# Optimization experiments

Hardware: AMD Instinct MI355X
Metric: run time of the kernel (lower is better)

The kernel has to match this reference:

```python
import jax, jax.numpy as jnp
import numpy as np

B, S, D = 1, 4096, 768
H = 12
HD = D // H  # 64


def setup_inputs() -> dict:
    key = jax.random.key(0)
    ks = jax.random.split(key, 6)
    sd = 1.0 / np.sqrt(D)
    return {
        "inputs": jax.random.normal(ks[0], (B, S, D), dtype=jnp.float32),
        "Wq": jax.random.uniform(ks[1], (D, D), jnp.float32, -sd, sd),
        "Wk": jax.random.uniform(ks[2], (D, D), jnp.float32, -sd, sd),
        "Wv": jax.random.uniform(ks[3], (D, D), jnp.float32, -sd, sd),
        "Wo": jax.random.uniform(ks[4], (D, D), jnp.float32, -sd, sd),
        "bo": jax.random.uniform(ks[5], (D,), jnp.float32, -sd, sd),
    }


def reference(inputs, Wq, Wk, Wv, Wo, bo):
    b, n, _ = inputs.shape
    # Linear layers (torch Linear: x @ W.T); W stored as [d_out, d_in]-equivalent here as [D, D] applied via x @ W.T
    q = inputs @ Wq.T  # [b, n, D]
    k = inputs @ Wk.T
    v = inputs @ Wv.T
    # [b, H, n, HD]
    q = q.reshape(b, n, H, HD).transpose(0, 2, 1, 3)
    k = k.reshape(b, n, H, HD).transpose(0, 2, 1, 3)
    v = v.reshape(b, n, H, HD).transpose(0, 2, 1, 3)
    scores = jnp.einsum("bhqd,bhkd->bhqk", q, k)
    causal = jnp.triu(jnp.ones((n, n), dtype=bool), k=1)
    scores = jnp.where(causal, -jnp.inf, scores)
    attn = jax.nn.softmax(scores / np.sqrt(HD), axis=-1)  # dropout p=0.0 -> identity
    ctx = jnp.einsum("bhqk,bhkd->bhqd", attn, v)
    ctx = ctx.transpose(0, 2, 1, 3).reshape(b, n, D)
    return ctx @ Wo.T + bo
```

## Files before the change

kernel.cpp:

```cpp
#include <hip/hip_runtime.h>
#include <math.h>

static constexpr int S_LEN  = 4096;
static constexpr int DMODEL = 768;
static constexpr int NHEAD  = 12;
static constexpr int HDIM   = 64;

typedef __attribute__((ext_vector_type(8))) short   bf16x8;
typedef __attribute__((ext_vector_type(4))) float   f32x4;
typedef __attribute__((ext_vector_type(8))) unsigned short us8;

__device__ __forceinline__ unsigned short f2b(float f) {
  union { float f; unsigned int u; } v; v.f = f;
  unsigned int u = v.u;
  return (unsigned short)((u + 0x7fffu + ((u >> 16) & 1u)) >> 16);
}

__device__ __forceinline__ unsigned short f2b_fast(float f) {
  unsigned int u;
  asm("v_cvt_pk_bf16_f32 %0, %1, %2" : "=v"(u) : "v"(f), "v"(0.f));
  return (unsigned short)u;
}

__device__ __forceinline__ float dpp_max16(float x) {
  float y;
  y = __int_as_float(__builtin_amdgcn_mov_dpp(__float_as_int(x), 0xB1, 0xf, 0xf, true)); x = fmaxf(x, y);
  y = __int_as_float(__builtin_amdgcn_mov_dpp(__float_as_int(x), 0x4E, 0xf, 0xf, true)); x = fmaxf(x, y);
  y = __int_as_float(__builtin_amdgcn_mov_dpp(__float_as_int(x), 0x124, 0xf, 0xf, true)); x = fmaxf(x, y);
  y = __int_as_float(__builtin_amdgcn_mov_dpp(__float_as_int(x), 0x128, 0xf, 0xf, true)); x = fmaxf(x, y);
  return x;
}

__global__ __launch_bounds__(256)
void cvt_f2b_kern(const float* __restrict__ in, unsigned short* __restrict__ out, int n) {
  int i = (blockIdx.x * blockDim.x + threadIdx.x) * 8;
  if (i >= n) return;
  float4 a = *(const float4*)(in + i);
  float4 b = *(const float4*)(in + i + 4);
  ushort4 o0; o0.x = f2b(a.x); o0.y = f2b(a.y); o0.z = f2b(a.z); o0.w = f2b(a.w);
  ushort4 o1; o1.x = f2b(b.x); o1.y = f2b(b.y); o1.z = f2b(b.z); o1.w = f2b(b.w);
  *(ushort4*)(out + i)     = o0;
  *(ushort4*)(out + i + 4) = o1;
}

__global__ __launch_bounds__(256)
void cvt_f2b4_kern(const float* __restrict__ s0, const float* __restrict__ s1,
                   const float* __restrict__ s2, const float* __restrict__ s3,
                   unsigned short* __restrict__ d0, unsigned short* __restrict__ d1,
                   unsigned short* __restrict__ d2, unsigned short* __restrict__ d3,
                   int n) {
  const float* s; unsigned short* d;
  switch (blockIdx.y) {
    case 0: s = s0; d = d0; break;
    case 1: s = s1; d = d1; break;
    case 2: s = s2; d = d2; break;
    default: s = s3; d = d3; break;
  }
  int i = (blockIdx.x * blockDim.x + threadIdx.x) * 8;
  if (i >= n) return;
  float4 a = *(const float4*)(s + i);
  float4 b = *(const float4*)(s + i + 4);
  ushort4 o0; o0.x = f2b(a.x); o0.y = f2b(a.y); o0.z = f2b(a.z); o0.w = f2b(a.w);
  ushort4 o1; o1.x = f2b(b.x); o1.y = f2b(b.y); o1.z = f2b(b.z); o1.w = f2b(b.w);
  *(ushort4*)(d + i)     = o0;
  *(ushort4*)(d + i + 4) = o1;
}

__global__ __launch_bounds__(256)
void transpose_bf16(const unsigned short* __restrict__ in, unsigned short* __restrict__ out) {
  __shared__ __align__(16) unsigned short Ts[64][72];
  const int d0 = blockIdx.x * 64, s0 = blockIdx.y * 64;
  const int r = threadIdx.x >> 2, q = threadIdx.x & 3;
#pragma unroll
  for (int hh = 0; hh < 2; ++hh) {
    const int c8 = q + hh * 4;
    us8 v = *(const us8*)(in + (size_t)(s0 + r) * DMODEL + d0 + c8 * 8);
    *(us8*)(&Ts[r][c8 * 8]) = v;
  }
  __syncthreads();
#pragma unroll
  for (int hh = 0; hh < 2; ++hh) {
    const int sq = q + hh * 4;
    __align__(16) unsigned short tmp[8];
#pragma unroll
    for (int j = 0; j < 8; ++j) tmp[j] = Ts[sq * 8 + j][r];
    *(us8*)(out + (size_t)(d0 + r) * S_LEN + s0 + sq * 8) = *(us8*)tmp;
  }
}

template<int OUT_MODE>
__device__ __forceinline__
void gemm_body(const unsigned short* __restrict__ A, const unsigned short* __restrict__ B,
               const float* __restrict__ bias, void* __restrict__ Cout,
               int M, int N, int K, float scale, int bx, int by,
               unsigned short* As, unsigned short* Bs) {
  const int l  = threadIdx.x & 63;
  const int w  = threadIdx.x >> 6;
  const int wm = (w >> 1) * 32, wn = (w & 1) * 32;
  const int m0 = by * 64;
  const int n0 = bx * 64;
  const int lr = l & 15, lg = l >> 4;
  const int sr = threadIdx.x >> 2, sq = threadIdx.x & 3;

  f32x4 acc[2][2] = {};
  us8 areg[2], breg[2];

#pragma unroll
  for (int p = 0; p < 2; ++p) {
    const int c = sq * 2 + p;
    areg[p] = *(const us8*)(A + (size_t)(m0 + sr) * K + c * 8);
    breg[p] = *(const us8*)(B + (size_t)(n0 + sr) * K + c * 8);
  }
#pragma unroll
  for (int p = 0; p < 2; ++p) {
    const int c = sq * 2 + p;
    const int slot = ((c ^ (sr & 7)) * 8);
    *(us8*)(&As[sr * 64 + slot]) = areg[p];
    *(us8*)(&Bs[sr * 64 + slot]) = breg[p];
  }
  __syncthreads();

  const int nsteps = K / 64;
  for (int t = 0; t < nsteps; ++t) {
    const bool more = (t + 1 < nsteps);
    if (more) {
      const int kn = (t + 1) * 64;
#pragma unroll
      for (int p = 0; p < 2; ++p) {
        const int c = sq * 2 + p;
        areg[p] = *(const us8*)(A + (size_t)(m0 + sr) * K + kn + c * 8);
        breg[p] = *(const us8*)(B + (size_t)(n0 + sr) * K + kn + c * 8);
      }
    }
#pragma unroll
    for (int kc = 0; kc < 2; ++kc) {
      const int cr = kc * 4 + lg;
      bf16x8 af[2], bfr[2];
#pragma unroll
      for (int mi = 0; mi < 2; ++mi) {
        const int row = wm + mi * 16 + lr;
        af[mi] = *(const bf16x8*)(&As[row * 64 + ((cr ^ (row & 7)) * 8)]);
      }
#pragma unroll
      for (int ni = 0; ni < 2; ++ni) {
        const int row = wn + ni * 16 + lr;
        bfr[ni] = *(const bf16x8*)(&Bs[row * 64 + ((cr ^ (row & 7)) * 8)]);
      }
#pragma unroll
      for (int mi = 0; mi < 2; ++mi)
#pragma unroll
        for (int ni = 0; ni < 2; ++ni)
          acc[mi][ni] = __builtin_amdgcn_mfma_f32_16x16x32_bf16(af[mi], bfr[ni], acc[mi][ni], 0, 0, 0);
    }
    __syncthreads();
    if (more) {
#pragma unroll
      for (int p = 0; p < 2; ++p) {
        const int c = sq * 2 + p;
        const int slot = ((c ^ (sr & 7)) * 8);
        *(us8*)(&As[sr * 64 + slot]) = areg[p];
        *(us8*)(&Bs[sr * 64 + slot]) = breg[p];
      }
      __syncthreads();
    }
  }

  const int orow = (l >> 4) * 4;
#pragma unroll
  for (int mi = 0; mi < 2; ++mi)
#pragma unroll
    for (int ni = 0; ni < 2; ++ni) {
      const int col = n0 + wn + ni * 16 + lr;
      float bb = (OUT_MODE == 1) ? bias[col] : 0.f;
#pragma unroll
      for (int r = 0; r < 4; ++r) {
        const int row = m0 + wm + mi * 16 + orow + r;
        float v = acc[mi][ni][r] * scale;
        if (OUT_MODE == 0)
          ((unsigned short*)Cout)[(size_t)row * N + col] = f2b(v);
        else
          ((float*)Cout)[(size_t)row * N + col] = v + bb;
      }
    }
}

__global__ __launch_bounds__(256)
void gemm_qkv_lds(const unsigned short* __restrict__ X,
                  const unsigned short* __restrict__ Wq, const unsigned short* __restrict__ Wk,
                  const unsigned short* __restrict__ Wv,
                  unsigned short* __restrict__ Qh, unsigned short* __restrict__ Kh,
                  unsigned short* __restrict__ Vh) {
  __shared__ __align__(16) unsigned short As[64 * 64];
  __shared__ __align__(16) unsigned short Bs[64 * 64];
  const unsigned short* B; unsigned short* C; float scale;
  switch (blockIdx.z) {
    case 0:  B = Wq; C = Qh; scale = 0.125f * 1.4426950408889634f; break;
    case 1:  B = Wk; C = Kh; scale = 1.0f;   break;
    default: B = Wv; C = Vh; scale = 1.0f;   break;
  }
  gemm_body<0>(X, B, nullptr, C, S_LEN, DMODEL, DMODEL, scale,
               blockIdx.x, blockIdx.y, As, Bs);
}

__global__ __launch_bounds__(256)
void gemm_lds_f32(const unsigned short* __restrict__ A, const unsigned short* __restrict__ B,
                  const float* __restrict__ bias, float* __restrict__ C) {
  __shared__ __align__(16) unsigned short As[64 * 64];
  __shared__ __align__(16) unsigned short Bs[64 * 64];
  gemm_body<1>(A, B, bias, C, S_LEN, DMODEL, DMODEL, 1.0f,
               blockIdx.x, blockIdx.y, As, Bs);
}

__global__ __launch_bounds__(256, 3)
void attn_fwd_mfma(const unsigned short* __restrict__ Q, const unsigned short* __restrict__ K,
                   const unsigned short* __restrict__ Vt, unsigned short* __restrict__ O) {
  __shared__ __align__(16) unsigned short Ks[2][64 * 64];
  __shared__ __align__(16) unsigned short Vs[2][64 * 64];
  __shared__ __align__(16) unsigned short Ps[4][2 * 16 * 64];

  const int item = blockIdx.x;
  int s;
  if (item < 256)      s = item;
  else if (item < 512) s = 767 - item;
  else                 s = item;
  const int qt = 63 - s / NHEAD;
  const int h  = s % NHEAD;
  const int q0 = qt * 64;
  const int tid = threadIdx.x;
  const int w = tid >> 6, l = tid & 63;
  const int lr = l & 15, lg = l >> 4;
  const int sr = tid >> 2, sq = tid & 3;

  const bf16x8 ones = {(short)0x3F80, (short)0x3F80, (short)0x3F80, (short)0x3F80,
                       (short)0x3F80, (short)0x3F80, (short)0x3F80, (short)0x3F80};

  bf16x8 qf[2];
#pragma unroll
  for (int kc = 0; kc < 2; ++kc)
    qf[kc] = *(const bf16x8*)(Q + (size_t)(q0 + w * 16 + lr) * DMODEL + h * HDIM + kc * 32 + lg * 8);

  f32x4 o_acc[4] = {};
  f32x4 l_acc = {};
  float m_i[4];
#pragma unroll
  for (int r = 0; r < 4; ++r) m_i[r] = -1e30f;

  const int nt2    = (qt + 2) >> 1;
  const int ntFull = (64 * qt >= 127) ? ((64 * qt - 127) / 128 + 1) : 0;

  us8 kreg[2][2], vreg[2][2];

#pragma unroll
  for (int hh = 0; hh < 2; ++hh)
#pragma unroll
    for (int p = 0; p < 2; ++p) {
      const int qw = sq * 2 + p;
      kreg[hh][p] = *(const us8*)(K  + (size_t)(hh * 64 + sr) * DMODEL + h * HDIM + qw * 8);
      vreg[hh][p] = *(const us8*)(Vt + (size_t)(h * HDIM + sr) * S_LEN + hh * 64 + qw * 8);
    }
#pragma unroll
  for (int hh = 0; hh < 2; ++hh)
#pragma unroll
    for (int p = 0; p < 2; ++p) {
      const int qw = sq * 2 + p;
      const int sw = (qw * 8) ^ ((sr & 7) * 8);
      *(us8*)(&Ks[hh][sr * 64 + sw]) = kreg[hh][p];
      *(us8*)(&Vs[hh][sr * 64 + sw]) = vreg[hh][p];
    }
  __syncthreads();

  for (int t = 0; t < nt2; ++t) {
    const int k0 = t * 128;
    const bool more = (t + 1 < nt2);
    const bool need_mask = (t >= ntFull);

    if (more) {
      const int k0n = k0 + 128;
#pragma unroll
      for (int hh = 0; hh < 2; ++hh)
#pragma unroll
        for (int p = 0; p < 2; ++p) {
          const int qw = sq * 2 + p;
          kreg[hh][p] = *(const us8*)(K  + (size_t)(k0n + hh * 64 + sr) * DMODEL + h * HDIM + qw * 8);
          vreg[hh][p] = *(const us8*)(Vt + (size_t)(h * HDIM + sr) * S_LEN + k0n + hh * 64 + qw * 8);
        }
    }

    f32x4 sacc[2][4] = {};
    __builtin_amdgcn_s_setprio(1);
#pragma unroll
    for (int hh = 0; hh < 2; ++hh)
#pragma unroll
      for (int kc = 0; kc < 2; ++kc)
#pragma unroll
        for (int cb = 0; cb < 4; ++cb) {
          const int kv = cb * 16 + lr;
          bf16x8 kf = *(const bf16x8*)(&Ks[hh][kv * 64 + ((kc * 32 + lg * 8) ^ ((kv & 7) * 8))]);
          sacc[hh][cb] = __builtin_amdgcn_mfma_f32_16x16x32_bf16(qf[kc], kf, sacc[hh][cb], 0, 0, 0);
        }
    __builtin_amdgcn_s_setprio(0);

    float sv[4][8], pm[4];
#pragma unroll
    for (int r = 0; r < 4; ++r) {
      const int qg = q0 + w * 16 + lg * 4 + r;
#pragma unroll
      for (int hh = 0; hh < 2; ++hh)
#pragma unroll
        for (int cb = 0; cb < 4; ++cb)
          sv[r][hh * 4 + cb] = sacc[hh][cb][r];
      if (need_mask) {
#pragma unroll
        for (int hh = 0; hh < 2; ++hh)
#pragma unroll
          for (int cb = 0; cb < 4; ++cb) {
            const int kg = k0 + hh * 64 + cb * 16 + lr;
            if (kg > qg) sv[r][hh * 4 + cb] = -1e30f;
          }
      }
      float mt = fmaxf(fmaxf(fmaxf(sv[r][0], sv[r][1]), fmaxf(sv[r][2], sv[r][3])),
                       fmaxf(fmaxf(sv[r][4], sv[r][5]), fmaxf(sv[r][6], sv[r][7])));
      pm[r] = dpp_max16(mt);
    }

    const int ok = (pm[0] <= m_i[0] + 8.f) && (pm[1] <= m_i[1] + 8.f) &&
                   (pm[2] <= m_i[2] + 8.f) && (pm[3] <= m_i[3] + 8.f);
    if (!__all(ok)) {
#pragma unroll
      for (int r = 0; r < 4; ++r) {
        const float mnew = fmaxf(m_i[r], pm[r]);
        const float alpha = __builtin_amdgcn_exp2f(m_i[r] - mnew);
        m_i[r] = mnew;
        l_acc[r] *= alpha;
#pragma unroll
        for (int db = 0; db < 4; ++db) o_acc[db][r] *= alpha;
      }
    }

    float p[4][8];
#pragma unroll
    for (int r = 0; r < 4; ++r)
#pragma unroll
      for (int e = 0; e < 8; ++e)
        p[r][e] = __builtin_amdgcn_exp2f(sv[r][e] - m_i[r]);

#pragma unroll
    for (int r = 0; r < 4; ++r) {
      const int qloc = lg * 4 + r;
#pragma unroll
      for (int hh = 0; hh < 2; ++hh)
#pragma unroll
        for (int cb = 0; cb < 4; ++cb) {
          const int kvl = cb * 16 + lr;
          Ps[w][hh * 1024 + qloc * 64 + (kvl ^ ((qloc & 7) * 8))] = f2b_fast(p[r][hh * 4 + cb]);
        }
    }

    __builtin_amdgcn_s_setprio(1);
#pragma unroll
    for (int hh = 0; hh < 2; ++hh)
#pragma unroll
      for (int kc = 0; kc < 2; ++kc) {
        bf16x8 pf = *(const bf16x8*)(&Ps[w][hh * 1024 + lr * 64 + ((kc * 32 + lg * 8) ^ ((lr & 7) * 8))]);
#pragma unroll
        for (int db = 0; db < 4; ++db) {
          const int d = db * 16 + lr;
          bf16x8 vf = *(const bf16x8*)(&Vs[hh][d * 64 + ((kc * 32 + lg * 8) ^ ((d & 7) * 8))]);
          o_acc[db] = __builtin_amdgcn_mfma_f32_16x16x32_bf16(pf, vf, o_acc[db], 0, 0, 0);
        }
        l_acc = __builtin_amdgcn_mfma_f32_16x16x32_bf16(pf, ones, l_acc, 0, 0, 0);
      }
    __builtin_amdgcn_s_setprio(0);

    __syncthreads();
    if (more) {
#pragma unroll
      for (int hh = 0; hh < 2; ++hh)
#pragma unroll
        for (int p = 0; p < 2; ++p) {
          const int qw = sq * 2 + p;
          const int sw = (qw * 8) ^ ((sr & 7) * 8);
          *(us8*)(&Ks[hh][sr * 64 + sw]) = kreg[hh][p];
          *(us8*)(&Vs[hh][sr * 64 + sw]) = vreg[hh][p];
        }
      __syncthreads();
    }
  }

#pragma unroll
  for (int r = 0; r < 4; ++r) {
    const float inv = 1.f / l_acc[r];
    const int row = q0 + w * 16 + lg * 4 + r;
#pragma unroll
    for (int db = 0; db < 4; ++db)
      O[(size_t)row * DMODEL + h * HDIM + db * 16 + lr] = f2b_fast(o_acc[db][r] * inv);
  }
}

extern "C" void kernel_launch(void* const* d_in, const int* in_sizes, int n_in,
                              void* d_out, int out_size, void* d_ws, size_t ws_size,
                              hipStream_t stream) {
  const float* x  = (const float*)d_in[0];
  const float* Wq = (const float*)d_in[1];
  const float* Wk = (const float*)d_in[2];
  const float* Wv = (const float*)d_in[3];
  const float* Wo = (const float*)d_in[4];
  const float* bo = (const float*)d_in[5];
  float* out = (float*)d_out;

  const size_t SD = (size_t)S_LEN * DMODEL;
  const size_t DD = (size_t)DMODEL * DMODEL;

  unsigned short* xh   = (unsigned short*)d_ws;
  unsigned short* Wqh  = xh   + SD;
  unsigned short* Wkh  = Wqh  + DD;
  unsigned short* Wvh  = Wkh  + DD;
  unsigned short* Woh  = Wvh  + DD;
  unsigned short* Qh   = Woh  + DD;
  unsigned short* Kh   = Qh   + SD;
  unsigned short* Vh   = Kh   + SD;
  unsigned short* Vth  = Vh   + SD;
  unsigned short* ctxh = Vth  + SD;

  const dim3 blk(256);

  cvt_f2b_kern<<<dim3((int)(SD / 8 / 256)), blk, 0, stream>>>(x, xh, (int)SD);
  cvt_f2b4_kern<<<dim3((int)(DD / 8 / 256), 4), blk, 0, stream>>>(
      Wq, Wk, Wv, Wo, Wqh, Wkh, Wvh, Woh, (int)DD);

  gemm_qkv_lds<<<dim3(DMODEL / 64, S_LEN / 64, 3), blk, 0, stream>>>(
      xh, Wqh, Wkh, Wvh, Qh, Kh, Vh);

  transpose_bf16<<<dim3(DMODEL / 64, S_LEN / 64), blk, 0, stream>>>(Vh, Vth);

  attn_fwd_mfma<<<dim3(S_LEN / 64 * NHEAD), blk, 0, stream>>>(Qh, Kh, Vth, ctxh);

  gemm_lds_f32<<<dim3(DMODEL / 64, S_LEN / 64), blk, 0, stream>>>(ctxh, Woh, bo, out);
}
```

Measured before the change: 135.0 us.

## Keep attention P in registers via transposed S MFMA and lane shuffles

Result: slower. 176.7 us (+30.9%).

```diff
diff --git a/kernel.cpp b/kernel.cpp
--- a/kernel.cpp
+++ b/kernel.cpp
@@ -21,14 +21,10 @@
   asm("v_cvt_pk_bf16_f32 %0, %1, %2" : "=v"(u) : "v"(f), "v"(0.f));
   return (unsigned short)u;
 }
-
-__device__ __forceinline__ float dpp_max16(float x) {
-  float y;
-  y = __int_as_float(__builtin_amdgcn_mov_dpp(__float_as_int(x), 0xB1, 0xf, 0xf, true)); x = fmaxf(x, y);
-  y = __int_as_float(__builtin_amdgcn_mov_dpp(__float_as_int(x), 0x4E, 0xf, 0xf, true)); x = fmaxf(x, y);
-  y = __int_as_float(__builtin_amdgcn_mov_dpp(__float_as_int(x), 0x124, 0xf, 0xf, true)); x = fmaxf(x, y);
-  y = __int_as_float(__builtin_amdgcn_mov_dpp(__float_as_int(x), 0x128, 0xf, 0xf, true)); x = fmaxf(x, y);
-  return x;
+__device__ __forceinline__ unsigned int cvt_pk(float lo, float hi) {
+  unsigned int u;
+  asm("v_cvt_pk_bf16_f32 %0, %1, %2" : "=v"(u) : "v"(lo), "v"(hi));
+  return u;
 }
 
 __global__ __launch_bounds__(256)
@@ -211,12 +207,11 @@
                blockIdx.x, blockIdx.y, As, Bs);
 }
 
-__global__ __launch_bounds__(256, 3)
+__global__ __launch_bounds__(256, 5)
 void attn_fwd_mfma(const unsigned short* __restrict__ Q, const unsigned short* __restrict__ K,
                    const unsigned short* __restrict__ Vt, unsigned short* __restrict__ O) {
   __shared__ __align__(16) unsigned short Ks[2][64 * 64];
   __shared__ __align__(16) unsigned short Vs[2][64 * 64];
-  __shared__ __align__(16) unsigned short Ps[4][2 * 16 * 64];
 
   const int item = blockIdx.x;
   int s;
@@ -230,9 +225,8 @@
   const int w = tid >> 6, l = tid & 63;
   const int lr = l & 15, lg = l >> 4;
   const int sr = tid >> 2, sq = tid & 3;
-
-  const bf16x8 ones = {(short)0x3F80, (short)0x3F80, (short)0x3F80, (short)0x3F80,
-                       (short)0x3F80, (short)0x3F80, (short)0x3F80, (short)0x3F80};
+  const bool hiP = (lg >= 2);
+  const bool hiQ = (lg & 1) != 0;
 
   bf16x8 qf[2];
 #pragma unroll
@@ -240,10 +234,8 @@
     qf[kc] = *(const bf16x8*)(Q + (size_t)(q0 + w * 16 + lr) * DMODEL + h * HDIM + kc * 32 + lg * 8);
 
   f32x4 o_acc[4] = {};
-  f32x4 l_acc = {};
-  float m_i[4];
-#pragma unroll
-  for (int r = 0; r < 4; ++r) m_i[r] = -1e30f;
+  float m_i = -1e30f, l_i = 0.f;
+  const int qg = q0 + w * 16 + lr;
 
   const int nt2    = (qt + 2) >> 1;
   const int ntFull = (64 * qt >= 127) ? ((64 * qt - 127) / 128 + 1) : 0;
@@ -296,80 +288,103 @@
         for (int cb = 0; cb < 4; ++cb) {
           const int kv = cb * 16 + lr;
           bf16x8 kf = *(const bf16x8*)(&Ks[hh][kv * 64 + ((kc * 32 + lg * 8) ^ ((kv & 7) * 8))]);
-          sacc[hh][cb] = __builtin_amdgcn_mfma_f32_16x16x32_bf16(qf[kc], kf, sacc[hh][cb], 0, 0, 0);
+          sacc[hh][cb] = __builtin_amdgcn_mfma_f32_16x16x32_bf16(kf, qf[kc], sacc[hh][cb], 0, 0, 0);
         }
     __builtin_amdgcn_s_setprio(0);
 
-    float sv[4][8], pm[4];
-#pragma unroll
-    for (int r = 0; r < 4; ++r) {
-      const int qg = q0 + w * 16 + lg * 4 + r;
+    if (need_mask) {
 #pragma unroll
       for (int hh = 0; hh < 2; ++hh)
 #pragma unroll
         for (int cb = 0; cb < 4; ++cb)
-          sv[r][hh * 4 + cb] = sacc[hh][cb][r];
-      if (need_mask) {
-#pragma unroll
-        for (int hh = 0; hh < 2; ++hh)
-#pragma unroll
-          for (int cb = 0; cb < 4; ++cb) {
-            const int kg = k0 + hh * 64 + cb * 16 + lr;
-            if (kg > qg) sv[r][hh * 4 + cb] = -1e30f;
+#pragma unroll
+          for (int r = 0; r < 4; ++r) {
+            const int kg = k0 + hh * 64 + cb * 16 + lg * 4 + r;
+            if (kg > qg) sacc[hh][cb][r] = -1e30f;
           }
-      }
-      float mt = fmaxf(fmaxf(fmaxf(sv[r][0], sv[r][1]), fmaxf(sv[r][2], sv[r][3])),
-                       fmaxf(fmaxf(sv[r][4], sv[r][5]), fmaxf(sv[r][6], sv[r][7])));
-      pm[r] = dpp_max16(mt);
-    }
-
-    const int ok = (pm[0] <= m_i[0] + 8.f) && (pm[1] <= m_i[1] + 8.f) &&
-                   (pm[2] <= m_i[2] + 8.f) && (pm[3] <= m_i[3] + 8.f);
+    }
+
+    float mx = -1e30f;
+#pragma unroll
+    for (int hh = 0; hh < 2; ++hh)
+#pragma unroll
+      for (int cb = 0; cb < 4; ++cb) {
+        float a = fmaxf(sacc[hh][cb][0], sacc[hh][cb][1]);
+        float b = fmaxf(sacc[hh][cb][2], sacc[hh][cb][3]);
+        mx = fmaxf(mx, fmaxf(a, b));
+      }
+    mx = fmaxf(mx, __shfl_xor(mx, 16));
+    mx = fmaxf(mx, __shfl_xor(mx, 32));
+
+    const int ok = (mx <= m_i + 8.f);
     if (!__all(ok)) {
-#pragma unroll
-      for (int r = 0; r < 4; ++r) {
-        const float mnew = fmaxf(m_i[r], pm[r]);
-        const float alpha = __builtin_amdgcn_exp2f(m_i[r] - mnew);
-        m_i[r] = mnew;
-        l_acc[r] *= alpha;
-#pragma unroll
-        for (int db = 0; db < 4; ++db) o_acc[db][r] *= alpha;
-      }
-    }
-
-    float p[4][8];
-#pragma unroll
-    for (int r = 0; r < 4; ++r)
-#pragma unroll
-      for (int e = 0; e < 8; ++e)
-        p[r][e] = __builtin_amdgcn_exp2f(sv[r][e] - m_i[r]);
-
-#pragma unroll
-    for (int r = 0; r < 4; ++r) {
-      const int qloc = lg * 4 + r;
-#pragma unroll
-      for (int hh = 0; hh < 2; ++hh)
-#pragma unroll
-        for (int cb = 0; cb < 4; ++cb) {
-          const int kvl = cb * 16 + lr;
-          Ps[w][hh * 1024 + qloc * 64 + (kvl ^ ((qloc & 7) * 8))] = f2b_fast(p[r][hh * 4 + cb]);
+      const float mnew = fmaxf(m_i, mx);
+      const float alpha = __builtin_amdgcn_exp2f(m_i - mnew);
+      m_i = mnew;
+      l_i *= alpha;
+      float ar[4];
+#pragma unroll
+      for (int r = 0; r < 4; ++r) ar[r] = __shfl(alpha, lg * 4 + r);
+#pragma unroll
+      for (int db = 0; db < 4; ++db)
+#pragma unroll
+        for (int r = 0; r < 4; ++r) o_acc[db][r] *= ar[r];
+    }
+
+    float p[8][4];
+    float rs = 0.f;
+#pragma unroll
+    for (int hh = 0; hh < 2; ++hh)
+#pragma unroll
+      for (int cb = 0; cb < 4; ++cb)
+#pragma unroll
+        for (int r = 0; r < 4; ++r) {
+          const float e = __builtin_amdgcn_exp2f(sacc[hh][cb][r] - m_i);
+          p[hh * 4 + cb][r] = e;
+          rs += e;
         }
-    }
+    rs += __shfl_xor(rs, 16);
+    rs += __shfl_xor(rs, 32);
+    l_i += rs;
+
+    unsigned int pk[8][2];
+#pragma unroll
+    for (int b = 0; b < 8; ++b) {
+      pk[b][0] = cvt_pk(p[b][0], p[b][1]);
+      pk[b][1] = cvt_pk(p[b][2], p[b][3]);
+    }
+
+    unsigned int z0[4][2], z1[4][2];
+#pragma unroll
+    for (int k = 0; k < 4; ++k)
+#pragma unroll
+      for (int v = 0; v < 2; ++v) {
+        const unsigned int x0 = pk[2 * k][v];
+        const unsigned int x1 = pk[2 * k + 1][v];
+        const unsigned int snd = hiP ? x0 : x1;
+        const unsigned int rcv = (unsigned int)__shfl_xor((int)snd, 32);
+        const unsigned int y0 = hiP ? rcv : x0;
+        const unsigned int y1 = hiP ? x1 : rcv;
+        const unsigned int s2 = hiQ ? y0 : y1;
+        const unsigned int r2 = (unsigned int)__shfl_xor((int)s2, 16);
+        z0[k][v] = hiQ ? r2 : y0;
+        z1[k][v] = hiQ ? y1 : r2;
+      }
 
     __builtin_amdgcn_s_setprio(1);
 #pragma unroll
-    for (int hh = 0; hh < 2; ++hh)
-#pragma unroll
-      for (int kc = 0; kc < 2; ++kc) {
-        bf16x8 pf = *(const bf16x8*)(&Ps[w][hh * 1024 + lr * 64 + ((kc * 32 + lg * 8) ^ ((lr & 7) * 8))]);
-#pragma unroll
-        for (int db = 0; db < 4; ++db) {
-          const int d = db * 16 + lr;
-          bf16x8 vf = *(const bf16x8*)(&Vs[hh][d * 64 + ((kc * 32 + lg * 8) ^ ((d & 7) * 8))]);
-          o_acc[db] = __builtin_amdgcn_mfma_f32_16x16x32_bf16(pf, vf, o_acc[db], 0, 0, 0);
-        }
-        l_acc = __builtin_amdgcn_mfma_f32_16x16x32_bf16(pf, ones, l_acc, 0, 0, 0);
-      }
+    for (int kc2 = 0; kc2 < 4; ++kc2) {
+      union { unsigned int u[4]; bf16x8 v; } pa;
+      pa.u[0] = z0[kc2][0]; pa.u[1] = z0[kc2][1];
+      pa.u[2] = z1[kc2][0]; pa.u[3] = z1[kc2][1];
+      const int hh = kc2 >> 1, kc = kc2 & 1;
+#pragma unroll
+      for (int db = 0; db < 4; ++db) {
+        const int d = db * 16 + lr;
+        bf16x8 vf = *(const bf16x8*)(&Vs[hh][d * 64 + ((kc * 32 + lg * 8) ^ ((d & 7) * 8))]);
+        o_acc[db] = __builtin_amdgcn_mfma_f32_16x16x32_bf16(pa.v, vf, o_acc[db], 0, 0, 0);
+      }
+    }
     __builtin_amdgcn_s_setprio(0);
 
     __syncthreads();
@@ -377,19 +392,22 @@
 #pragma unroll
       for (int hh = 0; hh < 2; ++hh)
 #pragma unroll
-        for (int p = 0; p < 2; ++p) {
-          const int qw = sq * 2 + p;
+        for (int p2 = 0; p2 < 2; ++p2) {
+          const int qw = sq * 2 + p2;
           const int sw = (qw * 8) ^ ((sr & 7) * 8);
-          *(us8*)(&Ks[hh][sr * 64 + sw]) = kreg[hh][p];
-          *(us8*)(&Vs[hh][sr * 64 + sw]) = vreg[hh][p];
+          *(us8*)(&Ks[hh][sr * 64 + sw]) = kreg[hh][p2];
+          *(us8*)(&Vs[hh][sr * 64 + sw]) = vreg[hh][p2];
         }
       __syncthreads();
     }
   }
 
+  float lrow[4];
+#pragma unroll
+  for (int r = 0; r < 4; ++r) lrow[r] = __shfl(l_i, lg * 4 + r);
 #pragma unroll
   for (int r = 0; r < 4; ++r) {
-    const float inv = 1.f / l_acc[r];
+    const float inv = 1.f / lrow[r];
     const int row = q0 + w * 16 + lg * 4 + r;
 #pragma unroll
     for (int db = 0; db < 4; ++db)
```
